# Kernel tuning notes

Hardware: AMD Instinct MI355X
Metric: run time of the kernel (lower is better)

## Reference

```python
import jax, jax.numpy as jnp
import numpy as np

T = 4096
FUTURE = 1024
IN = 2
H1, H2, H3 = 151, 251, 51
OUT = 2


def setup_inputs() -> dict:
    key = jax.random.key(0)
    ks = jax.random.split(key, 16)

    def p(k, shape, fan):
        s = 1.0 / np.sqrt(fan)  # torch LSTMCell/Linear uniform(-1/sqrt(h),1/sqrt(h)) init scale
        return jax.random.uniform(k, shape, dtype=jnp.float32, minval=-s, maxval=s)

    inp = {
        "x": jax.random.normal(ks[0], (1, T, IN), dtype=jnp.float32),
        "W_ih1": p(ks[1], (4 * H1, IN), H1),
        "W_hh1": p(ks[2], (4 * H1, H1), H1),
        "b_ih1": p(ks[3], (4 * H1,), H1),
        "b_hh1": p(ks[4], (4 * H1,), H1),
        "W_ih2": p(ks[5], (4 * H2, H1), H2),
        "W_hh2": p(ks[6], (4 * H2, H2), H2),
        "b_ih2": p(ks[7], (4 * H2,), H2),
        "b_hh2": p(ks[8], (4 * H2,), H2),
        "W_ih3": p(ks[9], (4 * H3, H2), H3),
        "W_hh3": p(ks[10], (4 * H3, H3), H3),
        "b_ih3": p(ks[11], (4 * H3,), H3),
        "b_hh3": p(ks[12], (4 * H3,), H3),
        "Wl": p(ks[13], (OUT, H3), H3),
        "bl": p(ks[14], (OUT,), H3),
        "future": FUTURE,
    }
    return inp


def _lstm_cell(x, h, c, Wih, Whh, bih, bhh):
    # gates order in torch LSTMCell: input, forget, cell(g), output
    gates = x @ Wih.T + bih + h @ Whh.T + bhh
    i, f, g, o = jnp.split(gates, 4, axis=-1)
    i = jax.nn.sigmoid(i)
    f = jax.nn.sigmoid(f)
    g = jnp.tanh(g)
    o = jax.nn.sigmoid(o)
    c = f * c + i * g
    h = o * jnp.tanh(c)
    return h, c


def reference(x, W_ih1, W_hh1, b_ih1, b_hh1, W_ih2, W_hh2, b_ih2, b_hh2,
              W_ih3, W_hh3, b_ih3, b_hh3, Wl, bl, future):
    dt = x.dtype

    def step(state, x_t):
        h1, c1, h2, c2, h3, c3 = state
        h1, c1 = _lstm_cell(x_t, h1, c1, W_ih1, W_hh1, b_ih1, b_hh1)
        h2, c2 = _lstm_cell(h1, h2, c2, W_ih2, W_hh2, b_ih2, b_hh2)
        h3, c3 = _lstm_cell(h2, h3, c3, W_ih3, W_hh3, b_ih3, b_hh3)
        y = h3 @ Wl.T + bl  # (1, 2)
        return (h1, c1, h2, c2, h3, c3), y

    z = lambda h: jnp.zeros((1, h), dtype=dt)
    state0 = (z(H1), z(H1), z(H2), z(H2), z(H3), z(H3))

    xs = jnp.swapaxes(x, 0, 1)  # (T, 1, IN)
    state, ys = jax.lax.scan(step, state0, xs)  # ys: (T, 1, 2)

    def fstep(carry, _):
        st, y = carry
        st2, y2 = step(st, y)  # feed previous output back as input
        return (st2, y2), y2

    (_, _), ys_f = jax.lax.scan(fstep, (state, ys[-1]), None, length=future)
    out = jnp.concatenate([ys, ys_f], axis=0)  # (T+future, 1, 2)
    return out.squeeze(1)  # (T+future, 2)
```

## Files before the change

kernel.cpp:

```cpp
#include <hip/hip_runtime.h>
#include <stdint.h>

#define T_MAIN 4096
#define T_TOT  5120

#define O_W2   0
#define O_W1   208896
#define O_W1B  249856
#define O_W3   257216
#define O_WY   289856
#define O_X    289920
#define O_H1T  294016
#define O_H2AT 1072408
#define O_H2BT 1717654

typedef _Float16 f16;
typedef _Float16 f16x2 __attribute__((ext_vector_type(2)));

__device__ __forceinline__ float fdot2(uint32_t a, uint32_t b, float c) {
  return __builtin_amdgcn_fdot2(__builtin_bit_cast(f16x2, a),
                                __builtin_bit_cast(f16x2, b), c, false);
}
__device__ __forceinline__ uint32_t packf16(float a, float b) {
  f16x2 p = { (_Float16)a, (_Float16)b };
  return __builtin_bit_cast(uint32_t, p);
}
__device__ __forceinline__ uint16_t f16bits(float v) {
  return __builtin_bit_cast(uint16_t, (_Float16)v);
}
__device__ __forceinline__ float sigm(float x) { return 1.f / (1.f + __expf(-x)); }
__device__ __forceinline__ float tanhfast(float x) { return 2.f / (1.f + __expf(-2.f * x)) - 1.f; }

__device__ float l2w(int pw, int tid, int s, const float* Wih2, const float* Whh2) {
  int NGU = pw ? 125 : 126;
  if (tid >= 4 * NGU) return 0.f;
  int g = tid / NGU, u = tid - g * NGU, ug = pw ? 126 + u : u;
  int R = g * 251 + ug;
  if (s < 151) return Wih2[R * 151 + s];
  if (s < 152) return 0.f;
  if (s < 280) { int j = s - 152; return (j < 126) ? Whh2[R * 251 + j] : 0.f; }
  if (s < 408) { int j = s - 280; return (j < 125) ? Whh2[R * 251 + 126 + j] : 0.f; }
  return 0.f;
}
__device__ float l3w(int r3, int s, const float* Wih3, const float* Whh3) {
  if (s < 128) { return (s < 126) ? Wih3[r3 * 251 + s] : 0.f; }
  if (s < 256) { int j = s - 128; return (j < 125) ? Wih3[r3 * 251 + 126 + j] : 0.f; }
  if (s < 320) { int j = s - 256; return (j < 51) ? Whh3[r3 * 51 + j] : 0.f; }
  return 0.f;
}

__global__ void prep(const float* __restrict__ x,
                     const float* __restrict__ Wih1, const float* __restrict__ Whh1,
                     const float* __restrict__ Wih2, const float* __restrict__ Whh2,
                     const float* __restrict__ Wih3, const float* __restrict__ Whh3,
                     const float* __restrict__ Wl,
                     uint32_t* __restrict__ ws) {
  int b = blockIdx.x, lt = threadIdx.x;
  if (b < 1024) {
    int pw = b >> 9, tid = b & 511;
    uint32_t* dst = ws + O_W2 + (size_t)(pw * 512 + tid) * 204;
    for (int d = lt; d < 204; d += 64)
      dst[d] = packf16(l2w(pw, tid, 2 * d, Wih2, Whh2),
                       l2w(pw, tid, 2 * d + 1, Wih2, Whh2));
  } else if (b < 1628) {
    int r = b - 1024;
    uint32_t* dst = ws + ((r < 512) ? (O_W1 + r * 80) : (O_W1B + (r - 512) * 80));
    for (int d = lt; d < 80; d += 64) {
      uint32_t v;
      if (d == 0)      v = packf16(Wih1[r * 2 + 0], Wih1[r * 2 + 1]);
      else if (d < 4)  v = 0u;
      else {
        int k0 = 2 * (d - 4), k1 = k0 + 1;
        v = packf16(k0 < 151 ? Whh1[r * 151 + k0] : 0.f,
                    k1 < 151 ? Whh1[r * 151 + k1] : 0.f);
      }
      dst[d] = v;
    }
  } else if (b < 2036) {
    int idx = b - 1628, r3 = idx >> 1, h = idx & 1;
    uint32_t* dst = ws + O_W3 + idx * 80;
    for (int d = lt; d < 80; d += 64) {
      int s0 = h * 160 + 2 * d;
      dst[d] = packf16(l3w(r3, s0, Wih3, Whh3), l3w(r3, s0 + 1, Wih3, Whh3));
    }
  } else if (b == 2036) {
    for (int d = lt; d < 64; d += 64) {
      int r = d >> 5, s0 = (d & 31) * 2;
      float v0 = (s0 < 51) ? Wl[r * 51 + s0] : 0.f;
      float v1 = (s0 + 1 < 51) ? Wl[r * 51 + s0 + 1] : 0.f;
      ws[O_WY + d] = packf16(v0, v1);
    }
  } else if (b == 2037) {
    for (int i = lt; i < 152; i += 64) ws[O_H1T + i] = 0u;
    for (int i = lt; i < 126; i += 64) ws[O_H2AT + i] = 0u;
    for (int i = lt; i < 125; i += 64) ws[O_H2BT + i] = 0u;
  } else {
    int i = (b - 2038) * 64 + lt;
    if (i < T_MAIN) ws[O_X + i] = packf16(x[2 * i], x[2 * i + 1]);
  }
}

__device__ __forceinline__ uint32_t pollslot(uint32_t* p, uint32_t tag, volatile int* bail) {
  if (*bail) return 0u;
  tag &= 0xffffu;
  for (int i = 0; i < 4000000; ++i) {
    uint32_t v = __hip_atomic_load(p, __ATOMIC_RELAXED, __HIP_MEMORY_SCOPE_AGENT);
    if ((v & 0xffffu) == tag) return v;
    if ((i & 0xffff) == 0xffff && *bail) return 0u;
  }
  *bail = 1;
  return 0u;
}
__device__ __forceinline__ void pubslot(uint32_t* p, uint16_t bits, uint32_t tag) {
  __hip_atomic_store(p, ((uint32_t)bits << 16) | (tag & 0xffffu),
                     __ATOMIC_RELAXED, __HIP_MEMORY_SCOPE_AGENT);
}

__global__ __launch_bounds__(512, 2) __attribute__((amdgpu_waves_per_eu(2, 2)))
void lstm3(
    uint32_t* __restrict__ ws,
    const float* __restrict__ bih1, const float* __restrict__ bhh1,
    const float* __restrict__ bih2, const float* __restrict__ bhh2,
    const float* __restrict__ bih3, const float* __restrict__ bhh3,
    const float* __restrict__ bl, float* __restrict__ out) {
  const int wg = blockIdx.x, tid = threadIdx.x;
  __shared__ float G[604];
  __shared__ __align__(16) uint16_t Vbuf[408];
  __shared__ __align__(16) uint16_t h1L[152];
  __shared__ __align__(16) uint16_t Vb3[320];
  __shared__ uint32_t yL;
  __shared__ int bailS;
  if (tid == 0) { bailS = 0; yL = 0u; }

  if (wg >= 1) {
    const int pw = wg - 1;
    const int NGU = pw ? 125 : 126;
    const int NG = 4 * NGU;
    const int OWN = pw ? 280 : 152;
    const int REM = pw ? 152 : 280;
    const int NREM = pw ? 126 : 125;
    uint32_t* const ownT = ws + (pw ? O_H2BT : O_H2AT);
    uint32_t* const remT = ws + (pw ? O_H2AT : O_H2BT);
    const int ownStr = pw ? 125 : 126;
    const int remStr = pw ? 126 : 125;

    uint32_t W2r[204];
    {
      const uint32_t* src = ws + O_W2 + (size_t)(pw * 512 + tid) * 204;
#pragma unroll
      for (int i = 0; i < 204; ++i) W2r[i] = src[i];
    }
    float bias = 0.f;
    if (tid < NG) {
      int g = tid / NGU, u = tid - g * NGU, ug = pw ? 126 + u : u;
      int R = g * 251 + ug;
      bias = bih2[R] + bhh2[R];
    }
    float c2 = 0.f;
    if (tid < 408) Vbuf[tid] = 0;
    __syncthreads();

#pragma unroll 1
    for (int t = 0; t < T_TOT; ++t) {
      if (tid < 151) {
        uint32_t v = pollslot(ws + O_H1T + (size_t)(t + 1) * 152 + tid, (uint32_t)(t + 1), &bailS);
        Vbuf[tid] = (uint16_t)(v >> 16);
      } else if (tid >= 160 && tid < 160 + NREM) {
        int j = tid - 160;
        uint32_t v = pollslot(remT + (size_t)t * remStr + j, (uint32_t)t, &bailS);
        Vbuf[REM + j] = (uint16_t)(v >> 16);
      }
      __syncthreads();
      if (tid < NG) {
        const uint4* V = (const uint4*)Vbuf;
        float g0 = bias, g1 = 0.f, g2 = 0.f, g3 = 0.f;
#pragma unroll
        for (int j = 0; j < 51; ++j) {
          uint4 hv = V[j];
          g0 = fdot2(W2r[4 * j + 0], hv.x, g0);
          g1 = fdot2(W2r[4 * j + 1], hv.y, g1);
          g2 = fdot2(W2r[4 * j + 2], hv.z, g2);
          g3 = fdot2(W2r[4 * j + 3], hv.w, g3);
        }
        G[tid] = (g0 + g1) + (g2 + g3);
      }
      __syncthreads();
      if (tid < NGU) {
        float gi = sigm(G[tid]), gf = sigm(G[NGU + tid]);
        float gg = tanhfast(G[2 * NGU + tid]), go = sigm(G[3 * NGU + tid]);
        c2 = gf * c2 + gi * gg;
        uint16_t bits = f16bits(go * tanhfast(c2));
        Vbuf[OWN + tid] = bits;
        pubslot(ownT + (size_t)(t + 1) * ownStr + tid, bits, (uint32_t)(t + 1));
      }
      __syncthreads();
    }
    return;
  }

  uint32_t W1x, W1h[76], Wex[80];
  {
    const uint32_t* s1 = ws + O_W1 + (size_t)tid * 80;
    W1x = s1[0];
#pragma unroll
    for (int j = 0; j < 76; ++j) W1h[j] = s1[4 + j];
  }
#pragma unroll
  for (int j = 0; j < 80; ++j) Wex[j] = 0u;
  if (tid < 92) {
    const uint32_t* s2 = ws + O_W1B + (size_t)tid * 80;
    Wex[0] = s2[0];
#pragma unroll
    for (int j = 0; j < 76; ++j) Wex[1 + j] = s2[4 + j];
  } else if (tid == 92 || tid == 93) {
    const uint32_t* s2 = ws + O_WY + (size_t)(tid - 92) * 32;
#pragma unroll
    for (int j = 0; j < 32; ++j) Wex[j] = s2[j];
  } else if (tid >= 104) {
    const uint32_t* s2 = ws + O_W3 + (size_t)(tid - 104) * 80;
#pragma unroll
    for (int j = 0; j < 80; ++j) Wex[j] = s2[j];
  }
  float b1a = bih1[tid] + bhh1[tid];
  float b1b = (tid < 92) ? (bih1[512 + tid] + bhh1[512 + tid]) : 0.f;
  float b3 = 0.f;
  if (tid >= 104 && ((tid - 104) & 1) == 0) {
    int r3 = (tid - 104) >> 1;
    b3 = bih3[r3] + bhh3[r3];
  }
  float by = (tid == 92 || tid == 93) ? bl[tid - 92] : 0.f;
  float c1 = 0.f, c3 = 0.f;
  if (tid < 152) h1L[tid] = 0;
  if (tid < 320) Vb3[tid] = 0;
  __syncthreads();

#pragma unroll 1
  for (int t = 0; t < T_MAIN; ++t) {
    uint32_t xin = ws[O_X + t];
    const uint4* Hp = (const uint4*)h1L;
    {
      float g0 = fdot2(W1x, xin, b1a), g1 = 0.f, g2 = 0.f, g3 = 0.f;
#pragma unroll
      for (int j = 0; j < 19; ++j) {
        uint4 hv = Hp[j];
        g0 = fdot2(W1h[4 * j + 0], hv.x, g0);
        g1 = fdot2(W1h[4 * j + 1], hv.y, g1);
        g2 = fdot2(W1h[4 * j + 2], hv.z, g2);
        g3 = fdot2(W1h[4 * j + 3], hv.w, g3);
      }
      G[tid] = (g0 + g1) + (g2 + g3);
    }
    if (tid < 92) {
      float g0 = fdot2(Wex[0], xin, b1b), g1 = 0.f, g2 = 0.f, g3 = 0.f;
#pragma unroll
      for (int j = 0; j < 19; ++j) {
        uint4 hv = Hp[j];
        g0 = fdot2(Wex[1 + 4 * j], hv.x, g0);
        g1 = fdot2(Wex[2 + 4 * j], hv.y, g1);
        g2 = fdot2(Wex[3 + 4 * j], hv.z, g2);
        g3 = fdot2(Wex[4 + 4 * j], hv.w, g3);
      }
      G[512 + tid] = (g0 + g1) + (g2 + g3);
    }
    __syncthreads();
    if (tid < 151) {
      float gi = sigm(G[tid]), gf = sigm(G[151 + tid]);
      float gg = tanhfast(G[302 + tid]), go = sigm(G[453 + tid]);
      c1 = gf * c1 + gi * gg;
      uint16_t bits = f16bits(go * tanhfast(c1));
      h1L[tid] = bits;
      pubslot(ws + O_H1T + (size_t)(t + 1) * 152 + tid, bits, (uint32_t)(t + 1));
    }
    __syncthreads();
  }

#pragma unroll 1
  for (int t = 0; t < T_MAIN; ++t) {
    if (tid < 126) {
      uint32_t v = pollslot(ws + O_H2AT + (size_t)(t + 1) * 126 + tid, (uint32_t)(t + 1), &bailS);
      Vb3[tid] = (uint16_t)(v >> 16);
    } else if (tid >= 128 && tid < 253) {
      int j = tid - 128;
      uint32_t v = pollslot(ws + O_H2BT + (size_t)(t + 1) * 125 + j, (uint32_t)(t + 1), &bailS);
      Vb3[128 + j] = (uint16_t)(v >> 16);
    }
    __syncthreads();
    if (tid >= 104) {
      int it = tid - 104, r3 = it >> 1, hf = it & 1;
      const uint4* V = (const uint4*)Vb3 + hf * 20;
      float g0 = 0.f, g1 = 0.f, g2 = 0.f, g3 = 0.f;
#pragma unroll
      for (int j = 0; j < 20; ++j) {
        uint4 hv = V[j];
        g0 = fdot2(Wex[4 * j + 0], hv.x, g0);
        g1 = fdot2(Wex[4 * j + 1], hv.y, g1);
        g2 = fdot2(Wex[4 * j + 2], hv.z, g2);
        g3 = fdot2(Wex[4 * j + 3], hv.w, g3);
      }
      float s = (g0 + g1) + (g2 + g3);
      s += __shfl_xor(s, 1);
      if (!hf) G[r3] = s + b3;
    }
    __syncthreads();
    if (tid < 51) {
      float gi = sigm(G[tid]), gf = sigm(G[51 + tid]);
      float gg = tanhfast(G[102 + tid]), go = sigm(G[153 + tid]);
      c3 = gf * c3 + gi * gg;
      Vb3[256 + tid] = f16bits(go * tanhfast(c3));
    }
    __syncthreads();
    if (tid == 92 || tid == 93) {
      const uint4* V = (const uint4*)Vb3 + 32;
      float g0 = by, g1 = 0.f, g2 = 0.f, g3 = 0.f;
#pragma unroll
      for (int j = 0; j < 8; ++j) {
        uint4 hv = V[j];
        g0 = fdot2(Wex[4 * j + 0], hv.x, g0);
        g1 = fdot2(Wex[4 * j + 1], hv.y, g1);
        g2 = fdot2(Wex[4 * j + 2], hv.z, g2);
        g3 = fdot2(Wex[4 * j + 3], hv.w, g3);
      }
      float y = (g0 + g1) + (g2 + g3);
      out[2 * t + (tid - 92)] = y;
      float y1 = __shfl(y, 29);
      if (tid == 92) yL = packf16(y, y1);
    }
  }
  __syncthreads();

#pragma unroll 1
  for (int t = T_MAIN; t < T_TOT; ++t) {
    uint32_t xin = yL;
    const uint4* Hp = (const uint4*)h1L;
    {
      float g0 = fdot2(W1x, xin, b1a), g1 = 0.f, g2 = 0.f, g3 = 0.f;
#pragma unroll
      for (int j = 0; j < 19; ++j) {
        uint4 hv = Hp[j];
        g0 = fdot2(W1h[4 * j + 0], hv.x, g0);
        g1 = fdot2(W1h[4 * j + 1], hv.y, g1);
        g2 = fdot2(W1h[4 * j + 2], hv.z, g2);
        g3 = fdot2(W1h[4 * j + 3], hv.w, g3);
      }
      G[tid] = (g0 + g1) + (g2 + g3);
    }
    if (tid < 92) {
      float g0 = fdot2(Wex[0], xin, b1b), g1 = 0.f, g2 = 0.f, g3 = 0.f;
#pragma unroll
      for (int j = 0; j < 19; ++j) {
        uint4 hv = Hp[j];
        g0 = fdot2(Wex[1 + 4 * j], hv.x, g0);
        g1 = fdot2(Wex[2 + 4 * j], hv.y, g1);
        g2 = fdot2(Wex[3 + 4 * j], hv.z, g2);
        g3 = fdot2(Wex[4 + 4 * j], hv.w, g3);
      }
      G[512 + tid] = (g0 + g1) + (g2 + g3);
    }
    __syncthreads();
    if (tid < 151) {
      float gi = sigm(G[tid]), gf = sigm(G[151 + tid]);
      float gg = tanhfast(G[302 + tid]), go = sigm(G[453 + tid]);
      c1 = gf * c1 + gi * gg;
      uint16_t bits = f16bits(go * tanhfast(c1));
      h1L[tid] = bits;
      pubslot(ws + O_H1T + (size_t)(t + 1) * 152 + tid, bits, (uint32_t)(t + 1));
    }
    __syncthreads();
    if (tid < 126) {
      uint32_t v = pollslot(ws + O_H2AT + (size_t)(t + 1) * 126 + tid, (uint32_t)(t + 1), &bailS);
      Vb3[tid] = (uint16_t)(v >> 16);
    } else if (tid >= 128 && tid < 253) {
      int j = tid - 128;
      uint32_t v = pollslot(ws + O_H2BT + (size_t)(t + 1) * 125 + j, (uint32_t)(t + 1), &bailS);
      Vb3[128 + j] = (uint16_t)(v >> 16);
    }
    __syncthreads();
    if (tid >= 104) {
      int it = tid - 104, r3 = it >> 1, hf = it & 1;
      const uint4* V = (const uint4*)Vb3 + hf * 20;
      float g0 = 0.f, g1 = 0.f, g2 = 0.f, g3 = 0.f;
#pragma unroll
      for (int j = 0; j < 20; ++j) {
        uint4 hv = V[j];
        g0 = fdot2(Wex[4 * j + 0], hv.x, g0);
        g1 = fdot2(Wex[4 * j + 1], hv.y, g1);
        g2 = fdot2(Wex[4 * j + 2], hv.z, g2);
        g3 = fdot2(Wex[4 * j + 3], hv.w, g3);
      }
      float s = (g0 + g1) + (g2 + g3);
      s += __shfl_xor(s, 1);
      if (!hf) G[r3] = s + b3;
    }
    __syncthreads();
    if (tid < 51) {
      float gi = sigm(G[tid]), gf = sigm(G[51 + tid]);
      float gg = tanhfast(G[102 + tid]), go = sigm(G[153 + tid]);
      c3 = gf * c3 + gi * gg;
      Vb3[256 + tid] = f16bits(go * tanhfast(c3));
    }
    __syncthreads();
    if (tid == 92 || tid == 93) {
      const uint4* V = (const uint4*)Vb3 + 32;
      float g0 = by, g1 = 0.f, g2 = 0.f, g3 = 0.f;
#pragma unroll
      for (int j = 0; j < 8; ++j) {
        uint4 hv = V[j];
        g0 = fdot2(Wex[4 * j + 0], hv.x, g0);
        g1 = fdot2(Wex[4 * j + 1], hv.y, g1);
        g2 = fdot2(Wex[4 * j + 2], hv.z, g2);
        g3 = fdot2(Wex[4 * j + 3], hv.w, g3);
      }
      float y = (g0 + g1) + (g2 + g3);
      out[2 * t + (tid - 92)] = y;
      float y1 = __shfl(y, 29);
      if (tid == 92) yL = packf16(y, y1);
    }
    __syncthreads();
  }
}

extern "C" void kernel_launch(void* const* d_in, const int* in_sizes, int n_in,
                              void* d_out, int out_size, void* d_ws, size_t ws_size,
                              hipStream_t stream) {
  (void)in_sizes; (void)n_in; (void)out_size; (void)ws_size;
  const float* x    = (const float*)d_in[0];
  const float* Wih1 = (const float*)d_in[1];
  const float* Whh1 = (const float*)d_in[2];
  const float* bih1 = (const float*)d_in[3];
  const float* bhh1 = (const float*)d_in[4];
  const float* Wih2 = (const float*)d_in[5];
  const float* Whh2 = (const float*)d_in[6];
  const float* bih2 = (const float*)d_in[7];
  const float* bhh2 = (const float*)d_in[8];
  const float* Wih3 = (const float*)d_in[9];
  const float* Whh3 = (const float*)d_in[10];
  const float* bih3 = (const float*)d_in[11];
  const float* bhh3 = (const float*)d_in[12];
  const float* Wl   = (const float*)d_in[13];
  const float* bl   = (const float*)d_in[14];

  uint32_t* ws = (uint32_t*)d_ws;

  prep<<<2102, 64, 0, stream>>>(x, Wih1, Whh1, Wih2, Whh2, Wih3, Whh3, Wl, ws);
  lstm3<<<3, 512, 0, stream>>>(ws, bih1, bhh1, bih2, bhh2, bih3, bhh3, bl,
                               (float*)d_out);
}
```

Measured before the change: 14.41 ms.

## Hold weights in AGPRs and spread active workgroups across XCDs

Part of each thread's register-resident weight array is moved into accumulator registers (AGPRs) with explicit accvgpr write and read instructions. This relieves VGPR pressure and avoids spills for the large per-thread weight arrays. The launch grows to 24 blocks, and only blocks with index mod 8 equal to 1 do work. This apparently places the three active workgroups on separate XCDs or a chosen CU placement. The cost is extra accvgpr read instructions in the inner dot-product loops, and cross-XCD communication may add polling latency.

```diff
diff --git a/kernel.cpp b/kernel.cpp
--- a/kernel.cpp
+++ b/kernel.cpp
@@ -27,6 +27,16 @@
 }
 __device__ __forceinline__ uint16_t f16bits(float v) {
   return __builtin_bit_cast(uint16_t, (_Float16)v);
+}
+__device__ __forceinline__ uint32_t aput(uint32_t v) {
+  uint32_t a;
+  asm("v_accvgpr_write_b32 %0, %1" : "=a"(a) : "v"(v));
+  return a;
+}
+__device__ __forceinline__ uint32_t aget(uint32_t a) {
+  uint32_t v;
+  asm("v_accvgpr_read_b32 %0, %1" : "=v"(v) : "a"(a));
+  return v;
 }
 __device__ __forceinline__ float sigm(float x) { return 1.f / (1.f + __expf(-x)); }
 __device__ __forceinline__ float tanhfast(float x) { return 2.f / (1.f + __expf(-2.f * x)) - 1.f; }
@@ -116,14 +126,18 @@
                      __ATOMIC_RELAXED, __HIP_MEMORY_SCOPE_AGENT);
 }
 
-__global__ __launch_bounds__(512, 2) __attribute__((amdgpu_waves_per_eu(2, 2)))
+__global__ __attribute__((amdgpu_flat_work_group_size(512, 512),
+                          amdgpu_waves_per_eu(2, 2)))
 void lstm3(
     uint32_t* __restrict__ ws,
     const float* __restrict__ bih1, const float* __restrict__ bhh1,
     const float* __restrict__ bih2, const float* __restrict__ bhh2,
     const float* __restrict__ bih3, const float* __restrict__ bhh3,
     const float* __restrict__ bl, float* __restrict__ out) {
-  const int wg = blockIdx.x, tid = threadIdx.x;
+  const int bid = blockIdx.x;
+  if ((bid & 7) != 1) return;
+  const int wg = bid >> 3;
+  const int tid = threadIdx.x;
   __shared__ float G[604];
   __shared__ __align__(16) uint16_t Vbuf[408];
   __shared__ __align__(16) uint16_t h1L[152];
@@ -144,11 +158,14 @@
     const int ownStr = pw ? 125 : 126;
     const int remStr = pw ? 126 : 125;
 
-    uint32_t W2r[204];
+    uint32_t W2lo[100];
+    uint32_t W2hi[104];
     {
       const uint32_t* src = ws + O_W2 + (size_t)(pw * 512 + tid) * 204;
 #pragma unroll
-      for (int i = 0; i < 204; ++i) W2r[i] = src[i];
+      for (int i = 0; i < 100; ++i) W2lo[i] = src[i];
+#pragma unroll
+      for (int i = 0; i < 104; ++i) W2hi[i] = aput(src[100 + i]);
     }
     float bias = 0.f;
     if (tid < NG) {
@@ -175,12 +192,20 @@
         const uint4* V = (const uint4*)Vbuf;
         float g0 = bias, g1 = 0.f, g2 = 0.f, g3 = 0.f;
 #pragma unroll
-        for (int j = 0; j < 51; ++j) {
+        for (int j = 0; j < 25; ++j) {
           uint4 hv = V[j];
-          g0 = fdot2(W2r[4 * j + 0], hv.x, g0);
-          g1 = fdot2(W2r[4 * j + 1], hv.y, g1);
-          g2 = fdot2(W2r[4 * j + 2], hv.z, g2);
-          g3 = fdot2(W2r[4 * j + 3], hv.w, g3);
+          g0 = fdot2(W2lo[4 * j + 0], hv.x, g0);
+          g1 = fdot2(W2lo[4 * j + 1], hv.y, g1);
+          g2 = fdot2(W2lo[4 * j + 2], hv.z, g2);
+          g3 = fdot2(W2lo[4 * j + 3], hv.w, g3);
+        }
+#pragma unroll
+        for (int j = 25; j < 51; ++j) {
+          uint4 hv = V[j];
+          g0 = fdot2(aget(W2hi[4 * (j - 25) + 0]), hv.x, g0);
+          g1 = fdot2(aget(W2hi[4 * (j - 25) + 1]), hv.y, g1);
+          g2 = fdot2(aget(W2hi[4 * (j - 25) + 2]), hv.z, g2);
+          g3 = fdot2(aget(W2hi[4 * (j - 25) + 3]), hv.w, g3);
         }
         G[tid] = (g0 + g1) + (g2 + g3);
       }
@@ -198,28 +223,34 @@
     return;
   }
 
-  uint32_t W1x, W1h[76], Wex[80];
+  uint32_t W1x, W1h[76];
+  uint32_t Wex[80];
   {
     const uint32_t* s1 = ws + O_W1 + (size_t)tid * 80;
     W1x = s1[0];
 #pragma unroll
     for (int j = 0; j < 76; ++j) W1h[j] = s1[4 + j];
   }
-#pragma unroll
-  for (int j = 0; j < 80; ++j) Wex[j] = 0u;
-  if (tid < 92) {
-    const uint32_t* s2 = ws + O_W1B + (size_t)tid * 80;
-    Wex[0] = s2[0];
-#pragma unroll
-    for (int j = 0; j < 76; ++j) Wex[1 + j] = s2[4 + j];
-  } else if (tid == 92 || tid == 93) {
-    const uint32_t* s2 = ws + O_WY + (size_t)(tid - 92) * 32;
-#pragma unroll
-    for (int j = 0; j < 32; ++j) Wex[j] = s2[j];
-  } else if (tid >= 104) {
-    const uint32_t* s2 = ws + O_W3 + (size_t)(tid - 104) * 80;
-#pragma unroll
-    for (int j = 0; j < 80; ++j) Wex[j] = s2[j];
+  {
+    uint32_t tmp[80];
+#pragma unroll
+    for (int j = 0; j < 80; ++j) tmp[j] = 0u;
+    if (tid < 92) {
+      const uint32_t* s2 = ws + O_W1B + (size_t)tid * 80;
+      tmp[0] = s2[0];
+#pragma unroll
+      for (int j = 0; j < 76; ++j) tmp[1 + j] = s2[4 + j];
+    } else if (tid == 92 || tid == 93) {
+      const uint32_t* s2 = ws + O_WY + (size_t)(tid - 92) * 32;
+#pragma unroll
+      for (int j = 0; j < 32; ++j) tmp[j] = s2[j];
+    } else if (tid >= 104) {
+      const uint32_t* s2 = ws + O_W3 + (size_t)(tid - 104) * 80;
+#pragma unroll
+      for (int j = 0; j < 80; ++j) tmp[j] = s2[j];
+    }
+#pragma unroll
+    for (int j = 0; j < 80; ++j) Wex[j] = aput(tmp[j]);
   }
   float b1a = bih1[tid] + bhh1[tid];
   float b1b = (tid < 92) ? (bih1[512 + tid] + bhh1[512 + tid]) : 0.f;
@@ -251,14 +282,14 @@
       G[tid] = (g0 + g1) + (g2 + g3);
     }
     if (tid < 92) {
-      float g0 = fdot2(Wex[0], xin, b1b), g1 = 0.f, g2 = 0.f, g3 = 0.f;
+      float g0 = fdot2(aget(Wex[0]), xin, b1b), g1 = 0.f, g2 = 0.f, g3 = 0.f;
 #pragma unroll
       for (int j = 0; j < 19; ++j) {
         uint4 hv = Hp[j];
-        g0 = fdot2(Wex[1 + 4 * j], hv.x, g0);
-        g1 = fdot2(Wex[2 + 4 * j], hv.y, g1);
-        g2 = fdot2(Wex[3 + 4 * j], hv.z, g2);
-        g3 = fdot2(Wex[4 + 4 * j], hv.w, g3);
+        g0 = fdot2(aget(Wex[1 + 4 * j]), hv.x, g0);
+        g1 = fdot2(aget(Wex[2 + 4 * j]), hv.y, g1);
+        g2 = fdot2(aget(Wex[3 + 4 * j]), hv.z, g2);
+        g3 = fdot2(aget(Wex[4 + 4 * j]), hv.w, g3);
       }
       G[512 + tid] = (g0 + g1) + (g2 + g3);
     }
@@ -292,10 +323,10 @@
 #pragma unroll
       for (int j = 0; j < 20; ++j) {
         uint4 hv = V[j];
-        g0 = fdot2(Wex[4 * j + 0], hv.x, g0);
-        g1 = fdot2(Wex[4 * j + 1], hv.y, g1);
-        g2 = fdot2(Wex[4 * j + 2], hv.z, g2);
-        g3 = fdot2(Wex[4 * j + 3], hv.w, g3);
+        g0 = fdot2(aget(Wex[4 * j + 0]), hv.x, g0);
+        g1 = fdot2(aget(Wex[4 * j + 1]), hv.y, g1);
+        g2 = fdot2(aget(Wex[4 * j + 2]), hv.z, g2);
+        g3 = fdot2(aget(Wex[4 * j + 3]), hv.w, g3);
       }
       float s = (g0 + g1) + (g2 + g3);
       s += __shfl_xor(s, 1);
@@ -315,10 +346,10 @@
 #pragma unroll
       for (int j = 0; j < 8; ++j) {
         uint4 hv = V[j];
-        g0 = fdot2(Wex[4 * j + 0], hv.x, g0);
-        g1 = fdot2(Wex[4 * j + 1], hv.y, g1);
-        g2 = fdot2(Wex[4 * j + 2], hv.z, g2);
-        g3 = fdot2(Wex[4 * j + 3], hv.w, g3);
+        g0 = fdot2(aget(Wex[4 * j + 0]), hv.x, g0);
+        g1 = fdot2(aget(Wex[4 * j + 1]), hv.y, g1);
+        g2 = fdot2(aget(Wex[4 * j + 2]), hv.z, g2);
+        g3 = fdot2(aget(Wex[4 * j + 3]), hv.w, g3);
       }
       float y = (g0 + g1) + (g2 + g3);
       out[2 * t + (tid - 92)] = y;
@@ -345,14 +376,14 @@
       G[tid] = (g0 + g1) + (g2 + g3);
     }
     if (tid < 92) {
-      float g0 = fdot2(Wex[0], xin, b1b), g1 = 0.f, g2 = 0.f, g3 = 0.f;
+      float g0 = fdot2(aget(Wex[0]), xin, b1b), g1 = 0.f, g2 = 0.f, g3 = 0.f;
 #pragma unroll
       for (int j = 0; j < 19; ++j) {
         uint4 hv = Hp[j];
-        g0 = fdot2(Wex[1 + 4 * j], hv.x, g0);
-        g1 = fdot2(Wex[2 + 4 * j], hv.y, g1);
-        g2 = fdot2(Wex[3 + 4 * j], hv.z, g2);
-        g3 = fdot2(Wex[4 + 4 * j], hv.w, g3);
+        g0 = fdot2(aget(Wex[1 + 4 * j]), hv.x, g0);
+        g1 = fdot2(aget(Wex[2 + 4 * j]), hv.y, g1);
+        g2 = fdot2(aget(Wex[3 + 4 * j]), hv.z, g2);
+        g3 = fdot2(aget(Wex[4 + 4 * j]), hv.w, g3);
       }
       G[512 + tid] = (g0 + g1) + (g2 + g3);
     }
@@ -382,10 +413,10 @@
 #pragma unroll
       for (int j = 0; j < 20; ++j) {
         uint4 hv = V[j];
-        g0 = fdot2(Wex[4 * j + 0], hv.x, g0);
-        g1 = fdot2(Wex[4 * j + 1], hv.y, g1);
-        g2 = fdot2(Wex[4 * j + 2], hv.z, g2);
-        g3 = fdot2(Wex[4 * j + 3], hv.w, g3);
+        g0 = fdot2(aget(Wex[4 * j + 0]), hv.x, g0);
+        g1 = fdot2(aget(Wex[4 * j + 1]), hv.y, g1);
+        g2 = fdot2(aget(Wex[4 * j + 2]), hv.z, g2);
+        g3 = fdot2(aget(Wex[4 * j + 3]), hv.w, g3);
       }
       float s = (g0 + g1) + (g2 + g3);
       s += __shfl_xor(s, 1);
@@ -405,10 +436,10 @@
 #pragma unroll
       for (int j = 0; j < 8; ++j) {
         uint4 hv = V[j];
-        g0 = fdot2(Wex[4 * j + 0], hv.x, g0);
-        g1 = fdot2(Wex[4 * j + 1], hv.y, g1);
-        g2 = fdot2(Wex[4 * j + 2], hv.z, g2);
-        g3 = fdot2(Wex[4 * j + 3], hv.w, g3);
+        g0 = fdot2(aget(Wex[4 * j + 0]), hv.x, g0);
+        g1 = fdot2(aget(Wex[4 * j + 1]), hv.y, g1);
+        g2 = fdot2(aget(Wex[4 * j + 2]), hv.z, g2);
+        g3 = fdot2(aget(Wex[4 * j + 3]), hv.w, g3);
       }
       float y = (g0 + g1) + (g2 + g3);
       out[2 * t + (tid - 92)] = y;
@@ -442,6 +473,6 @@
   uint32_t* ws = (uint32_t*)d_ws;
 
   prep<<<2102, 64, 0, stream>>>(x, Wih1, Whh1, Wih2, Whh2, Wih3, Whh3, Wl, ws);
-  lstm3<<<3, 512, 0, stream>>>(ws, bih1, bhh1, bih2, bhh2, bih3, bhh3, bl,
-                               (float*)d_out);
-}
+  lstm3<<<24, 512, 0, stream>>>(ws, bih1, bhh1, bih2, bhh2, bih3, bhh3, bl,
+                                (float*)d_out);
+}
```

New measurement: 18.13 ms. 25.8% more time.
